# Kernel tuning notes

Hardware: AMD Instinct MI355X
Metric: run time of the kernel (lower is better)

Reference implementation:

```python
import jax, jax.numpy as jnp
import numpy as np

H, W = 128, 128          # HT grid size
S = 16384                # sphere bins
V = 1_000_000            # num_votes
B, C = 4, 64


def setup_inputs() -> dict:
    key = jax.random.key(0)
    k1, k2, k3, k4 = jax.random.split(key, 4)
    x = jax.random.normal(k1, (B, C, H, W), dtype=jnp.float32)
    ht_idx = jax.random.randint(k2, (V,), 0, H * W)          # flattened HT cell index
    sph_idx = jax.random.randint(k3, (V,), 0, S)             # sphere bin index
    weight = jax.random.uniform(k4, (V,), dtype=jnp.float32)  # vote weight
    vote_mapping = jnp.stack(
        [ht_idx.astype(jnp.float32), weight, sph_idx.astype(jnp.float32)], axis=1
    )  # [V, 3] float32, matching the torch buffer layout
    return {"input": x, "vote_mapping": vote_mapping, "sphere_size": S}


def reference(input, vote_mapping, sphere_size):
    # Faithful to ht2sphere_forward: for each vote v,
    #   out[b, c, sphere_idx[v]] += input[b, c, ht_idx[v]] * weight[v]
    b, c, h, w = input.shape
    ht_idx = vote_mapping[:, 0].astype(jnp.int32)   # [V]
    weight = vote_mapping[:, 1]                     # [V]
    sph_idx = vote_mapping[:, 2].astype(jnp.int32)  # [V]
    flat = input.reshape(b * c, h * w)              # [BC, HW]
    vals = flat[:, ht_idx] * weight                 # [BC, V] gathered, weighted votes
    out = jax.ops.segment_sum(vals.T, sph_idx, num_segments=sphere_size)  # [S, BC]
    return out.T.reshape(b, c, sphere_size)
```

## Files before the change

kernel.cpp:

```cpp
#include <hip/hip_runtime.h>
#include <hip/hip_fp16.h>

#define HW_SZ 16384
#define S_SZ  16384
#define SEG_CAP 128
#define NBLK 256
#define INV_STEP 21.0f
#define STEP (1.0f / 21.0f)

typedef float f32x4 __attribute__((ext_vector_type(4)));

__global__ __launch_bounds__(1024)
void quant_hist_kernel(const float* __restrict__ x, unsigned char* __restrict__ xq,
                       const float* __restrict__ vm, unsigned char* __restrict__ hist8,
                       int V) {
    __shared__ __align__(16) int shmem[16384];
    const int tid = threadIdx.x;
    if (blockIdx.x < 256) {
        float (*tile)[32][33] = (float(*)[32][33])shmem;
        int sg = tid >> 8, t = tid & 255;
        int tx = t & 31, ty = t >> 5;
        for (int t4 = 0; t4 < 4; ++t4) {
            int tile_id = blockIdx.x * 16 + sg * 4 + t4;
            int by = tile_id >> 9, bx = tile_id & 511;
            __syncthreads();
#pragma unroll
            for (int j = 0; j < 32; j += 8)
                tile[sg][ty + j][tx] = __builtin_nontemporal_load(
                    &x[(size_t)(by * 32 + ty + j) * HW_SZ + bx * 32 + tx]);
            __syncthreads();
#pragma unroll
            for (int j = 0; j < 32; j += 8) {
                int ht = bx * 32 + ty + j, bc = by * 32 + tx;
                int q = (int)rintf(tile[sg][tx][ty + j] * INV_STEP);
                q = min(127, max(-127, q)) + 128;
                xq[(size_t)ht * 256 + bc] = (unsigned char)q;
            }
        }
    } else {
        int hb = blockIdx.x - 256;
        int* h = shmem;
        int4* h4 = (int4*)h;
        for (int i = tid; i < S_SZ / 4; i += 1024) h4[i] = make_int4(0, 0, 0, 0);
        __syncthreads();
        const float4* vm4 = (const float4*)vm;
        int nchunk4 = (V + 3) >> 2;
        int per = (nchunk4 + NBLK - 1) / NBLK;
        int cbeg = hb * per;
        int cend = min(nchunk4, cbeg + per);
        for (int g = cbeg + tid; g < cend; g += 1024) {
            float4 f0 = vm4[3 * g + 0];
            float4 f1 = vm4[3 * g + 1];
            float4 f2 = vm4[3 * g + 2];
            float spf[4] = {f0.z, f1.y, f2.x, f2.w};
            int vbase = g * 4;
#pragma unroll
            for (int j = 0; j < 4; ++j)
                if (vbase + j < V) atomicAdd(&h[(int)spf[j]], 1);
        }
        __syncthreads();
        unsigned char* hrow = hist8 + (size_t)hb * S_SZ;
        for (int i = tid; i < S_SZ / 4; i += 1024) {
            int4 v = h4[i];
            ((uchar4*)hrow)[i] = make_uchar4((unsigned char)v.x, (unsigned char)v.y,
                                             (unsigned char)v.z, (unsigned char)v.w);
        }
    }
}

__global__ __launch_bounds__(256)
void prefix_kernel(const unsigned char* __restrict__ hist8,
                   unsigned char* __restrict__ off8, int* __restrict__ cnt) {
    __shared__ unsigned lt[NBLK * 64];
    const int tid = threadIdx.x;
    const int bin0 = blockIdx.x * 256;
    for (int i = tid; i < NBLK * 64; i += 256) {
        int bb = i >> 6, w = i & 63;
        lt[i] = *(const unsigned*)(hist8 + (size_t)bb * S_SZ + bin0 + (w << 2));
    }
    __syncthreads();
    const unsigned char* lb = (const unsigned char*)lt;
    int sum = 0;
#pragma unroll 8
    for (int bb = 0; bb < NBLK; ++bb) {
        int c = lb[bb * 256 + tid];
        off8[(size_t)bb * S_SZ + bin0 + tid] = (unsigned char)sum;
        sum += c;
    }
    cnt[bin0 + tid] = min(sum, SEG_CAP);
}

__global__ __launch_bounds__(1024)
void place_kernel(const float* __restrict__ vm, const unsigned char* __restrict__ off8,
                  unsigned* __restrict__ bins, int V) {
    __shared__ int cur[S_SZ];
    const int tid = threadIdx.x;
    const unsigned char* orow = off8 + (size_t)blockIdx.x * S_SZ;
    for (int i = tid; i < S_SZ / 4; i += 1024) {
        uchar4 o = ((const uchar4*)orow)[i];
        int b = i << 2;
        cur[b + 0] = ((b + 0) << 7) + o.x;
        cur[b + 1] = ((b + 1) << 7) + o.y;
        cur[b + 2] = ((b + 2) << 7) + o.z;
        cur[b + 3] = ((b + 3) << 7) + o.w;
    }
    __syncthreads();
    const float4* vm4 = (const float4*)vm;
    int nchunk4 = (V + 3) >> 2;
    int per = (nchunk4 + NBLK - 1) / NBLK;
    int cbeg = blockIdx.x * per;
    int cend = min(nchunk4, cbeg + per);
    for (int g = cbeg + tid; g < cend; g += 1024) {
        float4 f0 = vm4[3 * g + 0];
        float4 f1 = vm4[3 * g + 1];
        float4 f2 = vm4[3 * g + 2];
        float htf[4] = {f0.x, f0.w, f1.z, f2.y};
        float wf[4]  = {f0.y, f1.x, f1.w, f2.z};
        float spf[4] = {f0.z, f1.y, f2.x, f2.w};
        int vbase = g * 4;
#pragma unroll
        for (int j = 0; j < 4; ++j) {
            if (vbase + j < V) {
                int s = (int)spf[j];
                int pos = atomicAdd(&cur[s], 1);
                if (pos < ((s + 1) << 7))
                    bins[pos] = ((unsigned)(int)htf[j] << 16) |
                                (unsigned)__half_as_ushort(__float2half(wf[j] * STEP));
            }
        }
    }
}

__global__ __launch_bounds__(1024)
void accum_kernel(const unsigned char* __restrict__ xq,
                  const unsigned* __restrict__ bins,
                  const int* __restrict__ cnt, float* __restrict__ out) {
    __shared__ __align__(16) unsigned smem[8320];
    float* st = (float*)smem;
    const int tid = threadIdx.x;
    int wave = tid >> 6, lane = tid & 63;
    int s0 = blockIdx.x * 32 + wave * 2;

    int nseg[2];
    float acc[2][4], sw[2];
#pragma unroll
    for (int k = 0; k < 2; ++k) {
        int s = s0 + k;
        int n = cnt[s];
        nseg[k] = n;
        unsigned* sv = smem + (wave * 2 + k) * 136;
        const unsigned* bs = bins + ((size_t)s << 7);
        if (lane < n)      sv[lane]      = __builtin_nontemporal_load(bs + lane);
        if (lane + 64 < n) sv[lane + 64] = __builtin_nontemporal_load(bs + lane + 64);
        if (lane < 8) sv[n + lane] = 0;
    }

#pragma unroll
    for (int k = 0; k < 2; ++k) {
        int n = nseg[k];
        const unsigned* vp = smem + (wave * 2 + k) * 136;
        float a0 = 0.f, a1 = 0.f, a2 = 0.f, a3 = 0.f, s_w = 0.f;
        for (int i = 0; i < n; i += 8) {
            uint4 wa = *(const uint4*)(vp + i);
            uint4 wb = *(const uint4*)(vp + i + 4);
            unsigned wd[8] = {wa.x, wa.y, wa.z, wa.w, wb.x, wb.y, wb.z, wb.w};
            unsigned dd[8];
#pragma unroll
            for (int t = 0; t < 8; ++t)
                dd[t] = *(const unsigned*)(xq + ((size_t)(wd[t] >> 16) << 8) + (lane << 2));
#pragma unroll
            for (int t = 0; t < 8; ++t) {
                float w = __half2float(__ushort_as_half((unsigned short)(wd[t] & 0xFFFFu)));
                unsigned p0 = __builtin_amdgcn_perm(0x64646464u, dd[t], 0x04010400u);
                unsigned p1 = __builtin_amdgcn_perm(0x64646464u, dd[t], 0x04030402u);
                __half2 h0 = *(const __half2*)&p0;
                __half2 h1 = *(const __half2*)&p1;
                a0 += w * __half2float(h0.x); a1 += w * __half2float(h0.y);
                a2 += w * __half2float(h1.x); a3 += w * __half2float(h1.y);
                s_w += w;
            }
        }
        acc[k][0] = a0; acc[k][1] = a1; acc[k][2] = a2; acc[k][3] = a3; sw[k] = s_w;
    }

    __syncthreads();
#pragma unroll
    for (int k = 0; k < 2; ++k) {
        float bias = 1152.0f * sw[k];
        *(float4*)&st[(wave * 2 + k) * 260 + lane * 4] =
            make_float4(acc[k][0] - bias, acc[k][1] - bias,
                        acc[k][2] - bias, acc[k][3] - bias);
    }
    __syncthreads();

#pragma unroll
    for (int r = 0; r < 2; ++r) {
        int ch = r * 128 + (tid >> 3);
        int i8 = tid & 7;
        f32x4 o = {st[(i8 * 4 + 0) * 260 + ch], st[(i8 * 4 + 1) * 260 + ch],
                   st[(i8 * 4 + 2) * 260 + ch], st[(i8 * 4 + 3) * 260 + ch]};
        __builtin_nontemporal_store(
            o, (f32x4*)(out + (size_t)ch * S_SZ + blockIdx.x * 32 + i8 * 4));
    }
}

extern "C" void kernel_launch(void* const* d_in, const int* in_sizes, int n_in,
                              void* d_out, int out_size, void* d_ws, size_t ws_size,
                              hipStream_t stream) {
    const float* x  = (const float*)d_in[0];
    const float* vm = (const float*)d_in[1];
    int V = in_sizes[1] / 3;
    float* out = (float*)d_out;

    char* ws = (char*)d_ws;
    unsigned char* xq    = (unsigned char*)(ws);
    unsigned*      bins  = (unsigned*)(ws + (4u << 20));
    unsigned char* hist8 = (unsigned char*)(ws + (12u << 20));
    unsigned char* off8  = (unsigned char*)(ws + (16u << 20));
    int*           cnt   = (int*)(ws + (20u << 20));

    quant_hist_kernel<<<512, 1024, 0, stream>>>(x, xq, vm, hist8, V);
    prefix_kernel<<<S_SZ / 256, 256, 0, stream>>>(hist8, off8, cnt);
    place_kernel<<<NBLK, 1024, 0, stream>>>(vm, off8, bins, V);
    accum_kernel<<<S_SZ / 32, 1024, 0, stream>>>(xq, bins, cnt, out);
}
```

Baseline: 136.1 us.

## Fuse prefix, place and accumulate kernels into one persistent kernel with grid barriers

Merges the prefix-sum, vote placement and accumulation stages into a single 256-block persistent kernel separated by software grid barriers on an atomic counter, removing two kernel launches and the gaps between them. The accumulation now has each block handle 64 sphere bins in two passes, and decodes the uint8 values with plain shifts and int-to-float conversion instead of the half-precision perm trick, adjusting the bias accordingly. This relies on all 256 blocks being co-resident for the spin barrier, and accumulation now runs on only 256 blocks instead of 512, which may reduce latency hiding.

```diff
diff --git a/kernel.cpp b/kernel.cpp
--- a/kernel.cpp
+++ b/kernel.cpp
@@ -5,17 +5,31 @@
 #define S_SZ  16384
 #define SEG_CAP 128
 #define NBLK 256
+#define GRID2 256
 #define INV_STEP 21.0f
 #define STEP (1.0f / 21.0f)
 
 typedef float f32x4 __attribute__((ext_vector_type(4)));
+
+__device__ inline void grid_bar(int* bar, int target) {
+    __syncthreads();
+    if (threadIdx.x == 0) {
+        __threadfence();
+        __hip_atomic_fetch_add(bar, 1, __ATOMIC_RELAXED, __HIP_MEMORY_SCOPE_AGENT);
+        while (__hip_atomic_load(bar, __ATOMIC_RELAXED, __HIP_MEMORY_SCOPE_AGENT) < target)
+            __builtin_amdgcn_s_sleep(8);
+        __threadfence();
+    }
+    __syncthreads();
+}
 
 __global__ __launch_bounds__(1024)
 void quant_hist_kernel(const float* __restrict__ x, unsigned char* __restrict__ xq,
                        const float* __restrict__ vm, unsigned char* __restrict__ hist8,
-                       int V) {
+                       int V, int* __restrict__ bar) {
     __shared__ __align__(16) int shmem[16384];
     const int tid = threadIdx.x;
+    if (blockIdx.x == 0 && tid == 0) *bar = 0;
     if (blockIdx.x < 256) {
         float (*tile)[32][33] = (float(*)[32][33])shmem;
         int sg = tid >> 8, t = tid & 255;
@@ -68,139 +82,143 @@
     }
 }
 
-__global__ __launch_bounds__(256)
-void prefix_kernel(const unsigned char* __restrict__ hist8,
-                   unsigned char* __restrict__ off8, int* __restrict__ cnt) {
-    __shared__ unsigned lt[NBLK * 64];
+__global__ __launch_bounds__(1024, 4)
+void sort_accum_kernel(const float* __restrict__ vm,
+                       const unsigned char* __restrict__ hist8,
+                       unsigned char* __restrict__ off8, int* __restrict__ cnt,
+                       unsigned* __restrict__ bins,
+                       const unsigned char* __restrict__ xq,
+                       float* __restrict__ out, int V, int* __restrict__ bar) {
+    __shared__ __align__(16) int shmem[16384];
     const int tid = threadIdx.x;
-    const int bin0 = blockIdx.x * 256;
-    for (int i = tid; i < NBLK * 64; i += 256) {
-        int bb = i >> 6, w = i & 63;
-        lt[i] = *(const unsigned*)(hist8 + (size_t)bb * S_SZ + bin0 + (w << 2));
+
+    if (blockIdx.x < 64) {
+        unsigned* lt = (unsigned*)shmem;
+        const int bin0 = blockIdx.x * 256;
+        for (int i = tid; i < 16384; i += 1024) {
+            int bb = i >> 6, w = i & 63;
+            lt[i] = *(const unsigned*)(hist8 + (size_t)bb * S_SZ + bin0 + (w << 2));
+        }
     }
     __syncthreads();
-    const unsigned char* lb = (const unsigned char*)lt;
-    int sum = 0;
+    if (blockIdx.x < 64 && tid < 256) {
+        const unsigned char* lb = (const unsigned char*)shmem;
+        const int bin0 = blockIdx.x * 256;
+        int sum = 0;
 #pragma unroll 8
-    for (int bb = 0; bb < NBLK; ++bb) {
-        int c = lb[bb * 256 + tid];
-        off8[(size_t)bb * S_SZ + bin0 + tid] = (unsigned char)sum;
-        sum += c;
-    }
-    cnt[bin0 + tid] = min(sum, SEG_CAP);
-}
-
-__global__ __launch_bounds__(1024)
-void place_kernel(const float* __restrict__ vm, const unsigned char* __restrict__ off8,
-                  unsigned* __restrict__ bins, int V) {
-    __shared__ int cur[S_SZ];
-    const int tid = threadIdx.x;
-    const unsigned char* orow = off8 + (size_t)blockIdx.x * S_SZ;
-    for (int i = tid; i < S_SZ / 4; i += 1024) {
-        uchar4 o = ((const uchar4*)orow)[i];
-        int b = i << 2;
-        cur[b + 0] = ((b + 0) << 7) + o.x;
-        cur[b + 1] = ((b + 1) << 7) + o.y;
-        cur[b + 2] = ((b + 2) << 7) + o.z;
-        cur[b + 3] = ((b + 3) << 7) + o.w;
-    }
-    __syncthreads();
-    const float4* vm4 = (const float4*)vm;
-    int nchunk4 = (V + 3) >> 2;
-    int per = (nchunk4 + NBLK - 1) / NBLK;
-    int cbeg = blockIdx.x * per;
-    int cend = min(nchunk4, cbeg + per);
-    for (int g = cbeg + tid; g < cend; g += 1024) {
-        float4 f0 = vm4[3 * g + 0];
-        float4 f1 = vm4[3 * g + 1];
-        float4 f2 = vm4[3 * g + 2];
-        float htf[4] = {f0.x, f0.w, f1.z, f2.y};
-        float wf[4]  = {f0.y, f1.x, f1.w, f2.z};
-        float spf[4] = {f0.z, f1.y, f2.x, f2.w};
-        int vbase = g * 4;
-#pragma unroll
-        for (int j = 0; j < 4; ++j) {
-            if (vbase + j < V) {
-                int s = (int)spf[j];
-                int pos = atomicAdd(&cur[s], 1);
-                if (pos < ((s + 1) << 7))
-                    bins[pos] = ((unsigned)(int)htf[j] << 16) |
-                                (unsigned)__half_as_ushort(__float2half(wf[j] * STEP));
-            }
-        }
-    }
-}
-
-__global__ __launch_bounds__(1024)
-void accum_kernel(const unsigned char* __restrict__ xq,
-                  const unsigned* __restrict__ bins,
-                  const int* __restrict__ cnt, float* __restrict__ out) {
-    __shared__ __align__(16) unsigned smem[8320];
-    float* st = (float*)smem;
-    const int tid = threadIdx.x;
-    int wave = tid >> 6, lane = tid & 63;
-    int s0 = blockIdx.x * 32 + wave * 2;
-
-    int nseg[2];
-    float acc[2][4], sw[2];
-#pragma unroll
-    for (int k = 0; k < 2; ++k) {
-        int s = s0 + k;
-        int n = cnt[s];
-        nseg[k] = n;
-        unsigned* sv = smem + (wave * 2 + k) * 136;
-        const unsigned* bs = bins + ((size_t)s << 7);
-        if (lane < n)      sv[lane]      = __builtin_nontemporal_load(bs + lane);
-        if (lane + 64 < n) sv[lane + 64] = __builtin_nontemporal_load(bs + lane + 64);
-        if (lane < 8) sv[n + lane] = 0;
-    }
-
-#pragma unroll
-    for (int k = 0; k < 2; ++k) {
-        int n = nseg[k];
-        const unsigned* vp = smem + (wave * 2 + k) * 136;
-        float a0 = 0.f, a1 = 0.f, a2 = 0.f, a3 = 0.f, s_w = 0.f;
-        for (int i = 0; i < n; i += 8) {
-            uint4 wa = *(const uint4*)(vp + i);
-            uint4 wb = *(const uint4*)(vp + i + 4);
-            unsigned wd[8] = {wa.x, wa.y, wa.z, wa.w, wb.x, wb.y, wb.z, wb.w};
-            unsigned dd[8];
-#pragma unroll
-            for (int t = 0; t < 8; ++t)
-                dd[t] = *(const unsigned*)(xq + ((size_t)(wd[t] >> 16) << 8) + (lane << 2));
-#pragma unroll
-            for (int t = 0; t < 8; ++t) {
-                float w = __half2float(__ushort_as_half((unsigned short)(wd[t] & 0xFFFFu)));
-                unsigned p0 = __builtin_amdgcn_perm(0x64646464u, dd[t], 0x04010400u);
-                unsigned p1 = __builtin_amdgcn_perm(0x64646464u, dd[t], 0x04030402u);
-                __half2 h0 = *(const __half2*)&p0;
-                __half2 h1 = *(const __half2*)&p1;
-                a0 += w * __half2float(h0.x); a1 += w * __half2float(h0.y);
-                a2 += w * __half2float(h1.x); a3 += w * __half2float(h1.y);
-                s_w += w;
-            }
-        }
-        acc[k][0] = a0; acc[k][1] = a1; acc[k][2] = a2; acc[k][3] = a3; sw[k] = s_w;
-    }
-
-    __syncthreads();
-#pragma unroll
-    for (int k = 0; k < 2; ++k) {
-        float bias = 1152.0f * sw[k];
-        *(float4*)&st[(wave * 2 + k) * 260 + lane * 4] =
-            make_float4(acc[k][0] - bias, acc[k][1] - bias,
-                        acc[k][2] - bias, acc[k][3] - bias);
-    }
-    __syncthreads();
-
-#pragma unroll
-    for (int r = 0; r < 2; ++r) {
-        int ch = r * 128 + (tid >> 3);
-        int i8 = tid & 7;
-        f32x4 o = {st[(i8 * 4 + 0) * 260 + ch], st[(i8 * 4 + 1) * 260 + ch],
-                   st[(i8 * 4 + 2) * 260 + ch], st[(i8 * 4 + 3) * 260 + ch]};
-        __builtin_nontemporal_store(
-            o, (f32x4*)(out + (size_t)ch * S_SZ + blockIdx.x * 32 + i8 * 4));
+        for (int bb = 0; bb < NBLK; ++bb) {
+            int c = lb[bb * 256 + tid];
+            off8[(size_t)bb * S_SZ + bin0 + tid] = (unsigned char)sum;
+            sum += c;
+        }
+        cnt[bin0 + tid] = min(sum, SEG_CAP);
+    }
+    grid_bar(bar, GRID2);
+
+    {
+        int* cur = shmem;
+        const unsigned char* orow = off8 + (size_t)blockIdx.x * S_SZ;
+        for (int i = tid; i < S_SZ / 4; i += 1024) {
+            uchar4 o = ((const uchar4*)orow)[i];
+            int b = i << 2;
+            cur[b + 0] = ((b + 0) << 7) + o.x;
+            cur[b + 1] = ((b + 1) << 7) + o.y;
+            cur[b + 2] = ((b + 2) << 7) + o.z;
+            cur[b + 3] = ((b + 3) << 7) + o.w;
+        }
+        __syncthreads();
+        const float4* vm4 = (const float4*)vm;
+        int nchunk4 = (V + 3) >> 2;
+        int per = (nchunk4 + NBLK - 1) / NBLK;
+        int cbeg = blockIdx.x * per;
+        int cend = min(nchunk4, cbeg + per);
+        for (int g = cbeg + tid; g < cend; g += 1024) {
+            float4 f0 = vm4[3 * g + 0];
+            float4 f1 = vm4[3 * g + 1];
+            float4 f2 = vm4[3 * g + 2];
+            float htf[4] = {f0.x, f0.w, f1.z, f2.y};
+            float wf[4]  = {f0.y, f1.x, f1.w, f2.z};
+            float spf[4] = {f0.z, f1.y, f2.x, f2.w};
+            int vbase = g * 4;
+#pragma unroll
+            for (int j = 0; j < 4; ++j) {
+                if (vbase + j < V) {
+                    int s = (int)spf[j];
+                    int pos = atomicAdd(&cur[s], 1);
+                    if (pos < ((s + 1) << 7))
+                        bins[pos] = ((unsigned)(int)htf[j] << 16) |
+                                    (unsigned)__half_as_ushort(__float2half(wf[j] * STEP));
+                }
+            }
+        }
+    }
+    grid_bar(bar, 2 * GRID2);
+
+    {
+        unsigned* svm = (unsigned*)shmem;
+        float* st = (float*)shmem;
+        int wave = tid >> 6, lane = tid & 63;
+        for (int b = 0; b < 2; ++b) {
+            __syncthreads();
+            int s0 = blockIdx.x * 64 + b * 32 + wave * 2;
+            int nseg[2];
+            float acc[2][4], sw[2];
+#pragma unroll
+            for (int k = 0; k < 2; ++k) {
+                int s = s0 + k;
+                int n = cnt[s];
+                nseg[k] = n;
+                unsigned* sv = svm + (wave * 2 + k) * 136;
+                const unsigned* bs = bins + ((size_t)s << 7);
+                if (lane < n)      sv[lane]      = __builtin_nontemporal_load(bs + lane);
+                if (lane + 64 < n) sv[lane + 64] = __builtin_nontemporal_load(bs + lane + 64);
+                if (lane < 8) sv[n + lane] = 0;
+            }
+#pragma unroll
+            for (int k = 0; k < 2; ++k) {
+                int n = nseg[k];
+                const unsigned* vp = svm + (wave * 2 + k) * 136;
+                float a0 = 0.f, a1 = 0.f, a2 = 0.f, a3 = 0.f, s_w = 0.f;
+                for (int i = 0; i < n; i += 8) {
+                    uint4 wa = *(const uint4*)(vp + i);
+                    uint4 wb = *(const uint4*)(vp + i + 4);
+                    unsigned wd[8] = {wa.x, wa.y, wa.z, wa.w, wb.x, wb.y, wb.z, wb.w};
+                    unsigned dd[8];
+#pragma unroll
+                    for (int t = 0; t < 8; ++t)
+                        dd[t] = *(const unsigned*)(xq + ((size_t)(wd[t] >> 16) << 8) + (lane << 2));
+#pragma unroll
+                    for (int t = 0; t < 8; ++t) {
+                        float w = __half2float(__ushort_as_half((unsigned short)(wd[t] & 0xFFFFu)));
+                        unsigned d = dd[t];
+                        a0 += w * (float)(d & 0xFFu);
+                        a1 += w * (float)((d >> 8) & 0xFFu);
+                        a2 += w * (float)((d >> 16) & 0xFFu);
+                        a3 += w * (float)(d >> 24);
+                        s_w += w;
+                    }
+                }
+                acc[k][0] = a0; acc[k][1] = a1; acc[k][2] = a2; acc[k][3] = a3; sw[k] = s_w;
+            }
+            __syncthreads();
+#pragma unroll
+            for (int k = 0; k < 2; ++k) {
+                float bias = 128.0f * sw[k];
+                *(float4*)&st[(wave * 2 + k) * 260 + lane * 4] =
+                    make_float4(acc[k][0] - bias, acc[k][1] - bias,
+                                acc[k][2] - bias, acc[k][3] - bias);
+            }
+            __syncthreads();
+#pragma unroll
+            for (int r = 0; r < 2; ++r) {
+                int ch = r * 128 + (tid >> 3);
+                int i8 = tid & 7;
+                f32x4 o = {st[(i8 * 4 + 0) * 260 + ch], st[(i8 * 4 + 1) * 260 + ch],
+                           st[(i8 * 4 + 2) * 260 + ch], st[(i8 * 4 + 3) * 260 + ch]};
+                __builtin_nontemporal_store(
+                    o, (f32x4*)(out + (size_t)ch * S_SZ + blockIdx.x * 64 + b * 32 + i8 * 4));
+            }
+        }
     }
 }
 
@@ -218,9 +236,9 @@
     unsigned char* hist8 = (unsigned char*)(ws + (12u << 20));
     unsigned char* off8  = (unsigned char*)(ws + (16u << 20));
     int*           cnt   = (int*)(ws + (20u << 20));
-
-    quant_hist_kernel<<<512, 1024, 0, stream>>>(x, xq, vm, hist8, V);
-    prefix_kernel<<<S_SZ / 256, 256, 0, stream>>>(hist8, off8, cnt);
-    place_kernel<<<NBLK, 1024, 0, stream>>>(vm, off8, bins, V);
-    accum_kernel<<<S_SZ / 32, 1024, 0, stream>>>(xq, bins, cnt, out);
-}
+    int*           bar   = (int*)(ws + (21u << 20));
+
+    quant_hist_kernel<<<512, 1024, 0, stream>>>(x, xq, vm, hist8, V, bar);
+    sort_accum_kernel<<<GRID2, 1024, 0, stream>>>(vm, hist8, off8, cnt, bins, xq,
+                                                  out, V, bar);
+}
```

After: 179.5 us. 1.32x slower.
